# Kernel tuning notes

Hardware: AMD Instinct MI355X
Metric: run time of the kernel (lower is better)

Reference implementation:

```python
import jax, jax.numpy as jnp
import numpy as np

T, B, IN, H, L = 128, 512, 512, 512, 2


def setup_inputs() -> dict:
    key = jax.random.key(0)
    ks = jax.random.split(key, 8)
    inp = {
        "latent": jax.random.normal(ks[0], (T, B, IN), jnp.float32),
        "h0": jax.random.normal(ks[1], (L, B, H), jnp.float32),
        "c0": jax.random.normal(ks[2], (L, B, H), jnp.float32),
        "reset_mask": jax.random.randint(ks[3], (T, B), 0, 2, jnp.int32),
    }
    # LSTM params, torch layout: W_ih (4H, in), W_hh (4H, H), biases (4H,) init to 1
    for l in range(L):
        in_l = IN if l == 0 else H
        k1, k2 = jax.random.split(jax.random.fold_in(key, 100 + l))
        inp[f"W_ih{l}"] = jax.random.normal(k1, (4 * H, in_l), jnp.float32) / np.float32(np.sqrt(in_l))
        inp[f"W_hh{l}"] = jax.random.normal(k2, (4 * H, H), jnp.float32) / np.float32(np.sqrt(H))
        inp[f"b_ih{l}"] = jnp.ones((4 * H,), jnp.float32)
        inp[f"b_hh{l}"] = jnp.ones((4 * H,), jnp.float32)
    return inp


def _cell(x, h, c, W_ih, W_hh, b_ih, b_hh):
    # torch gate order: input, forget, cell(g), output
    gates = x @ W_ih.T + b_ih + h @ W_hh.T + b_hh  # (B, 4H)
    i, f, g, o = jnp.split(gates, 4, axis=-1)
    i = jax.nn.sigmoid(i)
    f = jax.nn.sigmoid(f)
    g = jnp.tanh(g)
    o = jax.nn.sigmoid(o)
    c_new = f * c + i * g
    h_new = o * jnp.tanh(c_new)
    return h_new, c_new


def reference(latent, h0, c0, reset_mask,
              W_ih0, W_hh0, b_ih0, b_hh0,
              W_ih1, W_hh1, b_ih1, b_hh1):
    def step(carry, xs):
        h, c = carry  # (L, B, H) each
        x_t, m_t = xs
        m = (m_t != 0)[None, :, None]  # (1, B, 1), broadcast over layers and H
        h = jnp.where(m, 0.0, h)
        c = jnp.where(m, 0.0, c)
        h0n, c0n = _cell(x_t, h[0], c[0], W_ih0, W_hh0, b_ih0, b_hh0)
        h1n, c1n = _cell(h0n, h[1], c[1], W_ih1, W_hh1, b_ih1, b_hh1)
        return (jnp.stack([h0n, h1n]), jnp.stack([c0n, c1n])), h1n

    (h_n, c_n), hidden = jax.lax.scan(step, (h0, c0), (latent, reset_mask))
    return hidden, h_n, c_n  # hidden: (T, B, H)
```

## Files before the change

kernel.cpp:

```cpp
#include <hip/hip_runtime.h>
#include <hip/hip_bf16.h>

typedef __hip_bfloat16 bf16;
typedef unsigned short u16;
typedef unsigned long long u64;
using frag  = __attribute__((ext_vector_type(8))) short;
using f32x4 = __attribute__((ext_vector_type(4))) float;

static constexpr int T_  = 128;
static constexpr int B_  = 512;
static constexpr int H_  = 512;
static constexpr int K_  = 512;
static constexpr int G4_ = 2048;
static constexpr int NWG = 256;

static constexpr size_t W_BYTES = 131072;
static constexpr size_t SMEM_BYTES = W_BYTES;


__global__ void k_f32_to_bf16_v4(const float4* __restrict__ src,
                                 ushort4* __restrict__ dst, int n4) {
  int i = blockIdx.x * blockDim.x + threadIdx.x;
  int stride = gridDim.x * blockDim.x;
  for (; i < n4; i += stride) {
    float4 v = src[i];
    ushort4 o;
    bf16 t0 = __float2bfloat16(v.x); o.x = *reinterpret_cast<u16*>(&t0);
    bf16 t1 = __float2bfloat16(v.y); o.y = *reinterpret_cast<u16*>(&t1);
    bf16 t2 = __float2bfloat16(v.z); o.z = *reinterpret_cast<u16*>(&t2);
    bf16 t3 = __float2bfloat16(v.w); o.w = *reinterpret_cast<u16*>(&t3);
    dst[i] = o;
  }
}

__global__ void k_bias(const float* __restrict__ bih0, const float* __restrict__ bhh0,
                       const float* __restrict__ bih1, const float* __restrict__ bhh1,
                       float* __restrict__ bsum0, float* __restrict__ bsum1) {
  int i = blockIdx.x * blockDim.x + threadIdx.x;
  if (i < G4_) {
    bsum0[i] = bih0[i] + bhh0[i];
    bsum1[i] = bih1[i] + bhh1[i];
  }
}

__global__ void k_init2(const float* __restrict__ h0,
                        u16* __restrict__ bufA0, u16* __restrict__ bufA1) {
  int i = blockIdx.x * blockDim.x + threadIdx.x;
  int n = B_ * H_;
  if (i < n) {
    bf16 a = __float2bfloat16(h0[i]);
    bf16 b = __float2bfloat16(h0[n + i]);
    bufA0[i] = *reinterpret_cast<u16*>(&a);
    bufA1[n + i] = *reinterpret_cast<u16*>(&b);
  }
}

__global__ void k_zero(int* p) {
  int i = blockIdx.x * blockDim.x + threadIdx.x;
  if (i < 256) p[i] = 0;
}

__global__ __launch_bounds__(512, 2)
void k_main(const u16* __restrict__ latb,
            const u16* __restrict__ W0i, const u16* __restrict__ W0h,
            const u16* __restrict__ W1i, const u16* __restrict__ W1h,
            const float* __restrict__ bs0, const float* __restrict__ bs1,
            const int* __restrict__ reset,
            const float* __restrict__ c0,
            u16* __restrict__ h0seq,
            u16* __restrict__ bufA0,
            u16* __restrict__ bufA1,
            float* __restrict__ hidden,
            float* __restrict__ hn,
            float* __restrict__ cn,
            int* __restrict__ arr) {
  extern __shared__ char smem_raw[];
  u16* wlds = (u16*)smem_raw;
  __shared__ float hstage[8][16][20];

  const int tid   = threadIdx.x;
  const int wg    = blockIdx.x;
  const int lb    = wg & 7;
  const int layer = lb >> 2;
  const int bg    = lb & 3;
  const int cg    = wg >> 3;
  const int hbase = cg * 16;
  const int rowbase = bg * 128;
  const int wave  = tid >> 6;
  const int lane  = tid & 63;
  const int r16   = lane & 15;
  const int kq    = lane >> 4;
  const int wrow_local = wave * 16;
  const int wrow0 = rowbase + wrow_local;

  const u16* Wih = layer ? W1i : W0i;
  const u16* Whh = layer ? W1h : W0h;
  const float* bs = layer ? bs1 : bs0;
  u16* bufA_self = layer ? bufA1 : bufA0;

  const int slotOwn  = (lane & 31) * 8 + bg;
  const int slotPair = (lane >> 1) * 8 + (lane & 1) * 4 + bg;

  for (int it = 0; it < 16; ++it) {
    int c = it * 512 + tid;
    int fb = c >> 6, l = c & 63;
    int ni = fb >> 5, kslot = fb & 31;
    int col = hbase + (l & 15);
    int klocal = (kslot & 15) * 32 + (l >> 4) * 8;
    const u16* M = (kslot < 16) ? Wih : Whh;
    const u16* src = M + (size_t)(ni * H_ + col) * K_ + klocal;
    *(float4*)(wlds + ((size_t)c) * 8) = *(const float4*)src;
  }

  float bias[4];
  #pragma unroll
  for (int g = 0; g < 4; ++g) bias[g] = bs[g * H_ + hbase + r16];

  float creg[4];
  #pragma unroll
  for (int j = 0; j < 4; ++j)
    creg[j] = c0[((size_t)layer * B_ + (wrow0 + kq * 4 + j)) * H_ + hbase + r16];

  __syncthreads();

  for (int p = 0; p <= T_; ++p) {
    if (p) { asm volatile("buffer_inv sc0" ::: "memory"); }

    const int t = layer ? (p - 1) : p;
    const bool active = (t >= 0 && t < T_);
    float hnew_r[4], cnew_r[4];

    if (active) {
      const u16* X  = layer ? (h0seq + (size_t)t * B_ * H_)
                            : (latb + (size_t)t * B_ * K_);
      const u16* Hp = bufA_self + (size_t)(p & 1) * B_ * H_;
      u16* HnA      = bufA_self + (size_t)((p + 1) & 1) * B_ * H_;

      const int* rst_t = reset + (size_t)t * B_;
      const int ra0 = rst_t[wrow0 + r16];
      const u16* x0  = X  + (size_t)(wrow0 + r16) * K_ + kq * 8;
      const u16* hp0 = Hp + (size_t)(wrow0 + r16) * H_ + kq * 8;

      f32x4 acc[4] = {};
      const frag zf = {};

      #pragma unroll
      for (int s = 0; s < 16; ++s) {
        frag a  = *reinterpret_cast<const frag*>(x0 + s * 32);
        frag ah = ra0 ? zf : *reinterpret_cast<const frag*>(hp0 + s * 32);
        #pragma unroll
        for (int ni = 0; ni < 4; ++ni) {
          frag bx = *reinterpret_cast<const frag*>(
              wlds + ((size_t)((ni * 32 + s) * 64 + lane)) * 8);
          frag bh = *reinterpret_cast<const frag*>(
              wlds + ((size_t)((ni * 32 + 16 + s) * 64 + lane)) * 8);
          acc[ni] = __builtin_amdgcn_mfma_f32_16x16x32_bf16(a,  bx, acc[ni], 0, 0, 0);
          acc[ni] = __builtin_amdgcn_mfma_f32_16x16x32_bf16(ah, bh, acc[ni], 0, 0, 0);
        }
      }

      #pragma unroll
      for (int j = 0; j < 4; ++j) {
        const int rstj = rst_t[wrow0 + kq * 4 + j];
        float gi = acc[0][j] + bias[0];
        float gf = acc[1][j] + bias[1];
        float gg = acc[2][j] + bias[2];
        float go = acc[3][j] + bias[3];
        float iv = 1.f / (1.f + __expf(-gi));
        float fv = 1.f / (1.f + __expf(-gf));
        float gv = 1.f - 2.f / (__expf(2.f * gg) + 1.f);
        float ov = 1.f / (1.f + __expf(-go));
        float ce = rstj ? 0.f : creg[j];
        float cnew = fv * ce + iv * gv;
        float hnew = ov * (1.f - 2.f / (__expf(2.f * cnew) + 1.f));
        creg[j] = cnew;
        cnew_r[j] = cnew;
        hnew_r[j] = hnew;
        hstage[wave][kq * 4 + j][r16] = hnew;
      }

      {
        const int prow = lane >> 2;
        const int pc4  = lane & 3;
        float4 v = *reinterpret_cast<const float4*>(&hstage[wave][prow][pc4 * 4]);
        bf16 b0 = __float2bfloat16(v.x), b1 = __float2bfloat16(v.y);
        bf16 b2 = __float2bfloat16(v.z), b3 = __float2bfloat16(v.w);
        u64 pk = (u64)*reinterpret_cast<u16*>(&b0)
               | ((u64)*reinterpret_cast<u16*>(&b1) << 16)
               | ((u64)*reinterpret_cast<u16*>(&b2) << 32)
               | ((u64)*reinterpret_cast<u16*>(&b3) << 48);
        const size_t hoff = (size_t)(wrow0 + prow) * H_ + hbase + pc4 * 4;
        *(u64*)(HnA + hoff) = pk;
        if (layer == 0) {
          __hip_atomic_store((u64*)(h0seq + (size_t)t * B_ * H_ + hoff), pk,
                             __ATOMIC_RELAXED, __HIP_MEMORY_SCOPE_AGENT);
        }
      }
    }

    if (p < T_) {
      asm volatile("s_waitcnt vmcnt(0)" ::: "memory");
      __syncthreads();
      if (tid == 0)
        __hip_atomic_store(arr + wg, p + 1, __ATOMIC_RELAXED, __HIP_MEMORY_SCOPE_AGENT);
    }

    if (active) {
      float* hidden_t = hidden + (size_t)t * B_ * H_;
      #pragma unroll
      for (int j = 0; j < 4; ++j) {
        const size_t off = (size_t)(wrow0 + kq * 4 + j) * H_ + hbase + r16;
        if (layer) hidden_t[off] = hnew_r[j];
        if (t == T_ - 1) {
          hn[(size_t)layer * B_ * H_ + off] = hnew_r[j];
          cn[(size_t)layer * B_ * H_ + off] = cnew_r[j];
        }
      }
    }

    if (p < T_) {
      if (wave == 0) {
        if (layer == 0) {
          while (__hip_atomic_load(arr + slotOwn, __ATOMIC_RELAXED,
                                   __HIP_MEMORY_SCOPE_AGENT) < p + 1)
            __builtin_amdgcn_s_sleep(2);
        } else {
          while (__hip_atomic_load(arr + slotPair, __ATOMIC_RELAXED,
                                   __HIP_MEMORY_SCOPE_AGENT) < p + 1)
            __builtin_amdgcn_s_sleep(2);
        }
      }
      __syncthreads();
    }
  }
}


extern "C" void kernel_launch(void* const* d_in, const int* in_sizes, int n_in,
                              void* d_out, int out_size, void* d_ws, size_t ws_size,
                              hipStream_t stream) {
  (void)in_sizes; (void)n_in; (void)out_size; (void)ws_size;

  const float* latent = (const float*)d_in[0];
  const float* h0in   = (const float*)d_in[1];
  const float* c0in   = (const float*)d_in[2];
  const int*   reset  = (const int*)d_in[3];
  const float* W_ih0  = (const float*)d_in[4];
  const float* W_hh0  = (const float*)d_in[5];
  const float* b_ih0  = (const float*)d_in[6];
  const float* b_hh0  = (const float*)d_in[7];
  const float* W_ih1  = (const float*)d_in[8];
  const float* W_hh1  = (const float*)d_in[9];
  const float* b_ih1  = (const float*)d_in[10];
  const float* b_hh1  = (const float*)d_in[11];

  float* out    = (float*)d_out;
  float* hidden = out;
  float* hn     = out + (size_t)T_ * B_ * H_;
  float* cn     = hn + (size_t)2 * B_ * H_;

  char* ws = (char*)d_ws;
  u16* latb  = (u16*)ws;
  u16* wih0b = latb + (size_t)T_ * B_ * K_;
  u16* whh0b = wih0b + (size_t)G4_ * K_;
  u16* wih1b = whh0b + (size_t)G4_ * K_;
  u16* whh1b = wih1b + (size_t)G4_ * K_;
  float* bsum0 = (float*)(whh1b + (size_t)G4_ * K_);
  float* bsum1 = bsum0 + G4_;
  u16* h0seq = (u16*)(bsum1 + G4_);
  u16* bufA0 = h0seq + (size_t)T_ * B_ * H_;
  u16* bufA1 = bufA0 + (size_t)2 * B_ * H_;
  int* arr   = (int*)(bufA1 + (size_t)2 * B_ * H_);

  int n_lat4 = T_ * B_ * K_ / 4;
  k_f32_to_bf16_v4<<<2048, 256, 0, stream>>>((const float4*)latent, (ushort4*)latb, n_lat4);
  int n_w4 = G4_ * K_ / 4;
  k_f32_to_bf16_v4<<<256, 256, 0, stream>>>((const float4*)W_ih0, (ushort4*)wih0b, n_w4);
  k_f32_to_bf16_v4<<<256, 256, 0, stream>>>((const float4*)W_hh0, (ushort4*)whh0b, n_w4);
  k_f32_to_bf16_v4<<<256, 256, 0, stream>>>((const float4*)W_ih1, (ushort4*)wih1b, n_w4);
  k_f32_to_bf16_v4<<<256, 256, 0, stream>>>((const float4*)W_hh1, (ushort4*)whh1b, n_w4);
  k_bias<<<(G4_ + 255) / 256, 256, 0, stream>>>(b_ih0, b_hh0, b_ih1, b_hh1, bsum0, bsum1);
  k_init2<<<(B_ * H_ + 255) / 256, 256, 0, stream>>>(h0in, bufA0, bufA1);
  k_zero<<<1, 256, 0, stream>>>(arr);

  hipFuncSetAttribute((const void*)k_main, hipFuncAttributeMaxDynamicSharedMemorySize,
                      (int)SMEM_BYTES);
  void* args[] = { (void*)&latb, (void*)&wih0b, (void*)&whh0b, (void*)&wih1b, (void*)&whh1b,
                   (void*)&bsum0, (void*)&bsum1, (void*)&reset, (void*)&c0in,
                   (void*)&h0seq, (void*)&bufA0, (void*)&bufA1,
                   (void*)&hidden, (void*)&hn, (void*)&cn, (void*)&arr };
  hipLaunchCooperativeKernel((void*)k_main, dim3(NWG), dim3(512), args,
                             (unsigned int)SMEM_BYTES, stream);
}
```

Baseline: 1.361 ms.

## Split input and recurrent GEMM halves across two wave groups per block

Doubles the block to 1024 threads so that waves 0-7 compute the x·W_ih contribution and waves 8-15 compute the h·W_hh contribution at the same time. Partial accumulators go through a new LDS exchange buffer, and the first group then finishes the gates and cell update. This shortens the serial MFMA chain per step on the recurrent critical path, at the cost of an extra __syncthreads, LDS traffic, more shared memory and a larger block.

```diff
diff --git a/kernel.cpp b/kernel.cpp
--- a/kernel.cpp
+++ b/kernel.cpp
@@ -15,7 +15,8 @@
 static constexpr int NWG = 256;
 
 static constexpr size_t W_BYTES = 131072;
-static constexpr size_t SMEM_BYTES = W_BYTES;
+static constexpr size_t X_BYTES = 32768;
+static constexpr size_t SMEM_BYTES = W_BYTES + X_BYTES;
 
 
 __global__ void k_f32_to_bf16_v4(const float4* __restrict__ src,
@@ -60,7 +61,7 @@
   if (i < 256) p[i] = 0;
 }
 
-__global__ __launch_bounds__(512, 2)
+__global__ __launch_bounds__(1024, 4)
 void k_main(const u16* __restrict__ latb,
             const u16* __restrict__ W0i, const u16* __restrict__ W0h,
             const u16* __restrict__ W1i, const u16* __restrict__ W1h,
@@ -75,8 +76,8 @@
             float* __restrict__ cn,
             int* __restrict__ arr) {
   extern __shared__ char smem_raw[];
-  u16* wlds = (u16*)smem_raw;
-  __shared__ float hstage[8][16][20];
+  u16*   wlds = (u16*)smem_raw;
+  float* xch  = (float*)(smem_raw + W_BYTES);
 
   const int tid   = threadIdx.x;
   const int wg    = blockIdx.x;
@@ -90,8 +91,9 @@
   const int lane  = tid & 63;
   const int r16   = lane & 15;
   const int kq    = lane >> 4;
-  const int wrow_local = wave * 16;
-  const int wrow0 = rowbase + wrow_local;
+  const int rt    = wave & 7;
+  const int hf    = wave >> 3;
+  const int wrow0 = rowbase + rt * 16;
 
   const u16* Wih = layer ? W1i : W0i;
   const u16* Whh = layer ? W1h : W0h;
@@ -101,8 +103,8 @@
   const int slotOwn  = (lane & 31) * 8 + bg;
   const int slotPair = (lane >> 1) * 8 + (lane & 1) * 4 + bg;
 
-  for (int it = 0; it < 16; ++it) {
-    int c = it * 512 + tid;
+  for (int it = 0; it < 8; ++it) {
+    int c = it * 1024 + tid;
     int fb = c >> 6, l = c & 63;
     int ni = fb >> 5, kslot = fb & 31;
     int col = hbase + (l & 15);
@@ -123,6 +125,8 @@
 
   __syncthreads();
 
+  float* mytile = xch + (size_t)rt * 1024;
+
   for (int p = 0; p <= T_; ++p) {
     if (p) { asm volatile("buffer_inv sc0" ::: "memory"); }
 
@@ -130,35 +134,54 @@
     const bool active = (t >= 0 && t < T_);
     float hnew_r[4], cnew_r[4];
 
+    f32x4 acc[4] = {};
+    const int* rst_t = reset + (size_t)t * B_;
+
     if (active) {
-      const u16* X  = layer ? (h0seq + (size_t)t * B_ * H_)
-                            : (latb + (size_t)t * B_ * K_);
-      const u16* Hp = bufA_self + (size_t)(p & 1) * B_ * H_;
-      u16* HnA      = bufA_self + (size_t)((p + 1) & 1) * B_ * H_;
-
-      const int* rst_t = reset + (size_t)t * B_;
-      const int ra0 = rst_t[wrow0 + r16];
-      const u16* x0  = X  + (size_t)(wrow0 + r16) * K_ + kq * 8;
-      const u16* hp0 = Hp + (size_t)(wrow0 + r16) * H_ + kq * 8;
-
-      f32x4 acc[4] = {};
-      const frag zf = {};
+      if (hf == 0) {
+        const u16* X = layer ? (h0seq + (size_t)t * B_ * H_)
+                             : (latb + (size_t)t * B_ * K_);
+        const u16* x0 = X + (size_t)(wrow0 + r16) * K_ + kq * 8;
+        #pragma unroll
+        for (int s = 0; s < 16; ++s) {
+          frag a = *reinterpret_cast<const frag*>(x0 + s * 32);
+          #pragma unroll
+          for (int ni = 0; ni < 4; ++ni) {
+            frag b = *reinterpret_cast<const frag*>(
+                wlds + ((size_t)((ni * 32 + s) * 64 + lane)) * 8);
+            acc[ni] = __builtin_amdgcn_mfma_f32_16x16x32_bf16(a, b, acc[ni], 0, 0, 0);
+          }
+        }
+      } else {
+        const u16* Hp = bufA_self + (size_t)(p & 1) * B_ * H_;
+        const u16* hp0 = Hp + (size_t)(wrow0 + r16) * H_ + kq * 8;
+        const int ra0 = rst_t[wrow0 + r16];
+        const frag zf = {};
+        #pragma unroll
+        for (int s = 0; s < 16; ++s) {
+          frag a = ra0 ? zf : *reinterpret_cast<const frag*>(hp0 + s * 32);
+          #pragma unroll
+          for (int ni = 0; ni < 4; ++ni) {
+            frag b = *reinterpret_cast<const frag*>(
+                wlds + ((size_t)((ni * 32 + 16 + s) * 64 + lane)) * 8);
+            acc[ni] = __builtin_amdgcn_mfma_f32_16x16x32_bf16(a, b, acc[ni], 0, 0, 0);
+          }
+        }
+        #pragma unroll
+        for (int ni = 0; ni < 4; ++ni)
+          *(f32x4*)(mytile + ((size_t)ni * 64 + lane) * 4) = acc[ni];
+      }
+    }
+    __syncthreads();
+
+    if (active && hf == 0) {
+      u16* HnA  = bufA_self + (size_t)((p + 1) & 1) * B_ * H_;
 
       #pragma unroll
-      for (int s = 0; s < 16; ++s) {
-        frag a  = *reinterpret_cast<const frag*>(x0 + s * 32);
-        frag ah = ra0 ? zf : *reinterpret_cast<const frag*>(hp0 + s * 32);
-        #pragma unroll
-        for (int ni = 0; ni < 4; ++ni) {
-          frag bx = *reinterpret_cast<const frag*>(
-              wlds + ((size_t)((ni * 32 + s) * 64 + lane)) * 8);
-          frag bh = *reinterpret_cast<const frag*>(
-              wlds + ((size_t)((ni * 32 + 16 + s) * 64 + lane)) * 8);
-          acc[ni] = __builtin_amdgcn_mfma_f32_16x16x32_bf16(a,  bx, acc[ni], 0, 0, 0);
-          acc[ni] = __builtin_amdgcn_mfma_f32_16x16x32_bf16(ah, bh, acc[ni], 0, 0, 0);
-        }
-      }
-
+      for (int ni = 0; ni < 4; ++ni)
+        acc[ni] += *(const f32x4*)(mytile + ((size_t)ni * 64 + lane) * 4);
+
+      float* hstg = mytile;
       #pragma unroll
       for (int j = 0; j < 4; ++j) {
         const int rstj = rst_t[wrow0 + kq * 4 + j];
@@ -176,13 +199,13 @@
         creg[j] = cnew;
         cnew_r[j] = cnew;
         hnew_r[j] = hnew;
-        hstage[wave][kq * 4 + j][r16] = hnew;
+        hstg[(kq * 4 + j) * 20 + r16] = hnew;
       }
 
       {
         const int prow = lane >> 2;
         const int pc4  = lane & 3;
-        float4 v = *reinterpret_cast<const float4*>(&hstage[wave][prow][pc4 * 4]);
+        float4 v = *reinterpret_cast<const float4*>(hstg + prow * 20 + pc4 * 4);
         bf16 b0 = __float2bfloat16(v.x), b1 = __float2bfloat16(v.y);
         bf16 b2 = __float2bfloat16(v.z), b3 = __float2bfloat16(v.w);
         u64 pk = (u64)*reinterpret_cast<u16*>(&b0)
@@ -205,7 +228,7 @@
         __hip_atomic_store(arr + wg, p + 1, __ATOMIC_RELAXED, __HIP_MEMORY_SCOPE_AGENT);
     }
 
-    if (active) {
+    if (active && hf == 0) {
       float* hidden_t = hidden + (size_t)t * B_ * H_;
       #pragma unroll
       for (int j = 0; j < 4; ++j) {
@@ -289,6 +312,6 @@
                    (void*)&bsum0, (void*)&bsum1, (void*)&reset, (void*)&c0in,
                    (void*)&h0seq, (void*)&bufA0, (void*)&bufA1,
                    (void*)&hidden, (void*)&hn, (void*)&cn, (void*)&arr };
-  hipLaunchCooperativeKernel((void*)k_main, dim3(NWG), dim3(512), args,
+  hipLaunchCooperativeKernel((void*)k_main, dim3(NWG), dim3(1024), args,
                              (unsigned int)SMEM_BYTES, stream);
 }
```

Result: slower. 1.423 ms (+4.6%).
